# Optimization experiments

Measured on AMD Instinct MI355X. Metric: run time of the kernel, lower is better.

The kernel has to match this reference:

```python
import jax, jax.numpy as jnp
import numpy as np

B, L, DIN, H, E, K = 64, 256, 768, 64, 8, 2
S = 16  # sqrt(L): token<->feature grid side
LOSS_COEF = 1e-2


def gelu(x):
    return jax.nn.gelu(x, approximate=False)  # torch nn.GELU (exact erf)


def cv_squared(v):
    v = v.astype(jnp.float32)
    return jnp.var(v, ddof=1) / (jnp.mean(v) ** 2 + 1e-10)


def setup_inputs() -> dict:
    key = jax.random.key(0)
    ks = jax.random.split(key, 16)
    rn = lambda k, shape, s=0.02: jax.random.normal(k, shape, jnp.float32) * s
    lap = jnp.array([[0., 1., 0.], [1., -4., 1.], [0., 1., 0.]], jnp.float32)
    return {
        "x": jax.random.normal(ks[0], (B, L, DIN), jnp.float32),
        "dte": jax.random.normal(ks[1], (B, L, DIN), jnp.float32),
        "w_gate": rn(ks[2], (L, E), 1.0),
        "W_exp": rn(ks[3], (E, DIN, H)), "b_exp": jnp.zeros((E, H), jnp.float32),
        "W_sh": rn(ks[4], (DIN, H)), "b_sh": jnp.zeros((H,), jnp.float32),
        "ln_g": jnp.ones((H,), jnp.float32), "ln_b": jnp.zeros((H,), jnp.float32),
        "W_px": rn(ks[5], (H, 2 * H)), "b_px": jnp.zeros((2 * H,), jnp.float32),
        "conv_sh": jnp.tile(lap[None, None], (H, 1, 1, 1)),  # depthwise Laplacian [H,1,3,3]
        "W_pxx": rn(ks[6], (H, H)), "b_pxx": jnp.zeros((H,), jnp.float32),
        "W_dte": rn(ks[7], (H, H)), "b_dte": jnp.zeros((H,), jnp.float32),
        "W_dteall": rn(ks[8], (H, H)), "b_dteall": jnp.zeros((H,), jnp.float32),
        "W_rgb": rn(ks[9], (DIN, H)), "b_rgb": jnp.zeros((H,), jnp.float32),
        "W_fx": rn(ks[10], (H, H)), "b_fx": jnp.zeros((H,), jnp.float32),
        "W_fmod": rn(ks[11], (H, H)), "b_fmod": jnp.zeros((H,), jnp.float32),
        "W_fxx": rn(ks[12], (H, H)), "b_fxx": jnp.zeros((H,), jnp.float32),
    }


def reference(x, dte, w_gate, W_exp, b_exp, W_sh, b_sh, ln_g, ln_b, W_px, b_px,
              conv_sh, W_pxx, b_pxx, W_dte, b_dte, W_dteall, b_dteall,
              W_rgb, b_rgb, W_fx, b_fx, W_fmod, b_fmod, W_fxx, b_fxx):
    # ---- top-k gating (clean logits; noisy_gating=False / eval) ----
    logits = dte.mean(-1) @ w_gate                     # [B,E]
    topv, topi = jax.lax.top_k(logits, K)
    topg = jax.nn.softmax(topv, axis=1)
    gates = jnp.zeros_like(logits).at[jnp.arange(B)[:, None], topi].set(topg)
    importance = gates.sum(0)
    load = (gates > 0).sum(0).astype(jnp.float32)
    loss = LOSS_COEF * (cv_squared(importance) + cv_squared(load))
    # ---- sparse dispatch / expert Linear / weighted combine (dense-equivalent) ----
    y = jnp.einsum('be,bld,edh->blh', gates, dte, W_exp) + (gates @ b_exp)[:, None, :]
    # ---- shared expert Linear + Shared block ----
    sh = dte @ W_sh + b_sh                             # [B,L,H]
    shortcut = sh
    t = (sh - sh.mean(-1, keepdims=True)) * jax.lax.rsqrt(sh.var(-1, keepdims=True) + 1e-6)
    t = t * ln_g + ln_b
    t = t @ W_px + b_px                                # [B,L,2H]
    t1, t2 = t[..., :H], t[..., H:]
    f = t1.transpose(0, 2, 1).reshape(B, H, S, S)      # token2feature
    f = jax.lax.conv_general_dilated(f, conv_sh, (1, 1), 'SAME', feature_group_count=H)
    t1 = f.reshape(B, H, L).transpose(0, 2, 1)         # feature2token
    sh = (gelu(t1) * t2) @ W_pxx + b_pxx + shortcut
    # ---- combine MoE and shared streams ----
    dte_tok = (y @ W_dte + b_dte) + (sh @ W_dteall + b_dteall)
    rgb_tok = x @ W_rgb + b_rgb
    # ---- Fusion (its self.norm was overwritten to GELU; token<->feature round-trip is identity) ----
    shortcut = rgb_tok
    a = gelu(rgb_tok) @ W_fx + b_fx
    m = gelu(dte_tok) @ W_fmod + b_fmod
    out = (gelu(m) * a) @ W_fxx + b_fxx + shortcut     # [B,L,H]
    return out, loss
```

## Files before the change

### kernel.cpp

```cpp
#include <hip/hip_runtime.h>
#include <math.h>

typedef unsigned short u16;
typedef unsigned int u32;
typedef __attribute__((ext_vector_type(8))) short bf16x8;
typedef __attribute__((ext_vector_type(4))) float f32x4;


__device__ __forceinline__ float bf2f(u16 u) {
    union { u32 i; float f; } x; x.i = ((u32)u) << 16; return x.f;
}
__device__ __forceinline__ u16 f2bf(float f) {
    union { float f; u32 i; } x; x.f = f;
    u32 i = x.i;
    return (u16)((i + 0x7fffu + ((i >> 16) & 1u)) >> 16);
}
__device__ __forceinline__ u32 pack2(float a, float b) {
    return (u32)f2bf(a) | ((u32)f2bf(b) << 16);
}
__device__ __forceinline__ float wsum(float v) {
    #pragma unroll
    for (int o = 1; o < 64; o <<= 1) v += __shfl_xor(v, o, 64);
    return v;
}
__device__ __forceinline__ float gelu_f(float x) {
    return 0.5f * x * (1.0f + erff(x * 0.70710678118654752440f));
}

__global__ __launch_bounds__(256) void k_gate_part(const float* __restrict__ dte,
                                                   const float* __restrict__ w_gate,
                                                   float* __restrict__ partial) {
    __shared__ float dmeanS[64];
    int p = blockIdx.x, tid = threadIdx.x, w = tid >> 6, lane = tid & 63;
    for (int i = 0; i < 16; i++) {
        int l = w * 16 + i;
        const float* pr = dte + ((size_t)p * 64 + l) * 768;
        float s = 0.f;
        #pragma unroll
        for (int j = 0; j < 3; j++) {
            float4 v = *(const float4*)(pr + (lane + j * 64) * 4);
            s += v.x + v.y + v.z + v.w;
        }
        s = wsum(s);
        if (lane == 0) dmeanS[l] = s * (1.f / 768.f);
    }
    __syncthreads();
    if (w == 0) {
        float dm = dmeanS[lane];
        int wl = (p & 3) * 64 + lane;
        #pragma unroll
        for (int e = 0; e < 8; e++) {
            float s = wsum(dm * w_gate[wl * 8 + e]);
            if (lane == 0) partial[p * 8 + e] = s;
        }
    }
}

__global__ __launch_bounds__(256) void k_gate_fin(const float* __restrict__ partial,
                                                  const float* __restrict__ b_exp,
                                                  int* __restrict__ topi,
                                                  float* __restrict__ topg,
                                                  float* __restrict__ bias_y,
                                                  float* __restrict__ loss_out) {
    __shared__ float gS[64 * 8];
    __shared__ int i0S[64], i1S[64];
    __shared__ float g0S[64], g1S[64];
    int tid = threadIdx.x;
    if (tid < 64) {
        float lg[8];
        #pragma unroll
        for (int e = 0; e < 8; e++)
            lg[e] = partial[(tid * 4 + 0) * 8 + e] + partial[(tid * 4 + 1) * 8 + e] +
                    partial[(tid * 4 + 2) * 8 + e] + partial[(tid * 4 + 3) * 8 + e];
        int i0 = 0; float v0 = lg[0];
        #pragma unroll
        for (int e = 1; e < 8; e++) if (lg[e] > v0) { v0 = lg[e]; i0 = e; }
        int i1 = -1; float v1 = -1e30f;
        #pragma unroll
        for (int e = 0; e < 8; e++) if (e != i0 && lg[e] > v1) { v1 = lg[e]; i1 = e; }
        if (i1 < 0) i1 = (i0 + 1) & 7;
        float e2 = expf(v1 - v0);
        float g0 = 1.f / (1.f + e2);
        float g1 = e2 / (1.f + e2);
        #pragma unroll
        for (int e = 0; e < 8; e++) gS[tid * 8 + e] = 0.f;
        gS[tid * 8 + i0] = g0;
        gS[tid * 8 + i1] = g1;
        i0S[tid] = i0; i1S[tid] = i1; g0S[tid] = g0; g1S[tid] = g1;
        topi[tid * 2] = i0; topi[tid * 2 + 1] = i1;
        topg[tid * 2] = g0; topg[tid * 2 + 1] = g1;
    }
    __syncthreads();
    for (int idx = tid; idx < 4096; idx += 256) {
        int b = idx >> 6, h = idx & 63;
        bias_y[idx] = g0S[b] * b_exp[i0S[b] * 64 + h] + g1S[b] * b_exp[i1S[b] * 64 + h];
    }
    if (tid < 64) {
        float g[8];
        #pragma unroll
        for (int e = 0; e < 8; e++) g[e] = gS[tid * 8 + e];
        float imp[8], ld[8];
        #pragma unroll
        for (int e = 0; e < 8; e++) {
            imp[e] = wsum(g[e]);
            ld[e]  = wsum(g[e] > 0.f ? 1.f : 0.f);
        }
        if (tid == 0) {
            float l = 0.f;
            {
                float s = 0.f;
                #pragma unroll
                for (int e = 0; e < 8; e++) s += imp[e];
                float mn = s / 8.f, v = 0.f;
                #pragma unroll
                for (int e = 0; e < 8; e++) { float d = imp[e] - mn; v += d * d; }
                l += (v / 7.f) / (mn * mn + 1e-10f);
            }
            {
                float s = 0.f;
                #pragma unroll
                for (int e = 0; e < 8; e++) s += ld[e];
                float mn = s / 8.f, v = 0.f;
                #pragma unroll
                for (int e = 0; e < 8; e++) { float d = ld[e] - mn; v += d * d; }
                l += (v / 7.f) / (mn * mn + 1e-10f);
            }
            loss_out[0] = 0.01f * l;
        }
    }
}

__global__ __launch_bounds__(256) void k_gemm3(const float* __restrict__ dte,
                                               const float* __restrict__ x,
                                               const float* __restrict__ W_sh,
                                               const float* __restrict__ b_sh,
                                               const float* __restrict__ W_exp,
                                               const int* __restrict__ topi,
                                               const float* __restrict__ topg,
                                               const float* __restrict__ bias_y,
                                               const float* __restrict__ W_rgb,
                                               const float* __restrict__ b_rgb,
                                               float* __restrict__ buf_sh,
                                               u16* __restrict__ buf_y,
                                               float* __restrict__ out_rgb) {
    __shared__ u16 As[64 * 72];
    __shared__ u16 Wt[64 * 72];
    int bid = blockIdx.x;
    int kind, row0;
    if (bid < 512) { kind = bid & 1; row0 = (bid >> 1) * 64; }
    else           { kind = 2;       row0 = (bid - 512) * 64; }
    int b = row0 >> 8;
    int tid = threadIdx.x, wv = tid >> 6, lane = tid & 63;
    int m = lane & 15, quad = lane >> 4;

    const float* A = (kind == 2) ? x : dte;
    const float* W0 = (kind == 2) ? W_rgb : W_sh;
    const float* W1 = W0;
    float g0 = 0.f, g1 = 0.f;
    if (kind == 1) {
        W0 = W_exp + (size_t)topi[2 * b] * 49152;
        W1 = W_exp + (size_t)topi[2 * b + 1] * 49152;
        g0 = topg[2 * b]; g1 = topg[2 * b + 1];
    }

    float4 pa[2][2];
    float  pw[16];
    const int a_r  = tid >> 3;
    const int a_k8 = (tid & 7) * 8;
    const int w_n  = tid & 63;
    const int w_k0 = (tid >> 6) * 16;

    auto loadA = [&](int kc) {
        #pragma unroll
        for (int j = 0; j < 2; j++) {
            const float* src = A + (size_t)(row0 + a_r + j * 32) * 768 + kc * 64 + a_k8;
            pa[j][0] = *(const float4*)(src);
            pa[j][1] = *(const float4*)(src + 4);
        }
    };
    auto loadW = [&](int kc) {
        if (kind == 1) {
            #pragma unroll
            for (int j = 0; j < 16; j++) {
                size_t off = (size_t)(kc * 64 + w_k0 + j) * 64 + w_n;
                pw[j] = g0 * W0[off] + g1 * W1[off];
            }
        } else {
            #pragma unroll
            for (int j = 0; j < 16; j++)
                pw[j] = W0[(size_t)(kc * 64 + w_k0 + j) * 64 + w_n];
        }
    };
    auto stageLDS = [&]() {
        #pragma unroll
        for (int j = 0; j < 2; j++) {
            uint4 d;
            d.x = pack2(pa[j][0].x, pa[j][0].y);
            d.y = pack2(pa[j][0].z, pa[j][0].w);
            d.z = pack2(pa[j][1].x, pa[j][1].y);
            d.w = pack2(pa[j][1].z, pa[j][1].w);
            *(uint4*)&As[(a_r + j * 32) * 72 + a_k8] = d;
        }
        uint4 d0, d1;
        d0.x = pack2(pw[0],  pw[1]);  d0.y = pack2(pw[2],  pw[3]);
        d0.z = pack2(pw[4],  pw[5]);  d0.w = pack2(pw[6],  pw[7]);
        d1.x = pack2(pw[8],  pw[9]);  d1.y = pack2(pw[10], pw[11]);
        d1.z = pack2(pw[12], pw[13]); d1.w = pack2(pw[14], pw[15]);
        *(uint4*)&Wt[w_n * 72 + w_k0]     = d0;
        *(uint4*)&Wt[w_n * 72 + w_k0 + 8] = d1;
    };

    f32x4 acc0 = {0.f, 0.f, 0.f, 0.f}, acc1 = acc0, acc2 = acc0, acc3 = acc0;

    loadA(0); loadW(0);
    for (int kc = 0; kc < 12; kc++) {
        __syncthreads();
        stageLDS();
        __syncthreads();
        if (kc < 11) { loadA(kc + 1); loadW(kc + 1); }
        const int ar = (wv * 16 + m) * 72;
        bf16x8 a0 = *(const bf16x8*)&As[ar + quad * 8];
        bf16x8 a1 = *(const bf16x8*)&As[ar + 32 + quad * 8];
        #pragma unroll
        for (int t = 0; t < 4; t++) {
            const int br = (t * 16 + m) * 72;
            bf16x8 b0 = *(const bf16x8*)&Wt[br + quad * 8];
            bf16x8 b1 = *(const bf16x8*)&Wt[br + 32 + quad * 8];
            f32x4* accp = (t == 0) ? &acc0 : (t == 1) ? &acc1 : (t == 2) ? &acc2 : &acc3;
            *accp = __builtin_amdgcn_mfma_f32_16x16x32_bf16(a0, b0, *accp, 0, 0, 0);
            *accp = __builtin_amdgcn_mfma_f32_16x16x32_bf16(a1, b1, *accp, 0, 0, 0);
        }
    }

    f32x4 accs[4] = {acc0, acc1, acc2, acc3};
    #pragma unroll
    for (int t = 0; t < 4; t++) {
        int col = t * 16 + m;
        float bias;
        if (kind == 0)      bias = b_sh[col];
        else if (kind == 1) bias = bias_y[b * 64 + col];
        else                bias = b_rgb[col];
        #pragma unroll
        for (int i = 0; i < 4; i++) {
            int r = row0 + wv * 16 + quad * 4 + i;
            float val = accs[t][i] + bias;
            if (kind == 0)      buf_sh[(size_t)r * 64 + col] = val;
            else if (kind == 1) buf_y[(size_t)r * 64 + col] = f2bf(val);
            else                out_rgb[(size_t)r * 64 + col] = val;
        }
    }
}

__global__ __launch_bounds__(256) void k_lnpx(const float* __restrict__ buf_sh,
                                              const float* __restrict__ ln_g,
                                              const float* __restrict__ ln_b,
                                              const float* __restrict__ W_px,
                                              const float* __restrict__ b_px,
                                              u16* __restrict__ t1, u16* __restrict__ t2) {
    __shared__ float T[32 * 68];
    __shared__ float Wpx[8192];
    int r0 = blockIdx.x * 32;
    int tid = threadIdx.x, w = tid >> 6, lane = tid & 63;
    #pragma unroll
    for (int j = 0; j < 8; j++) {
        int e4 = tid + j * 256;
        *(float4*)(Wpx + e4 * 4) = *(const float4*)(W_px + e4 * 4);
    }
    float lnG = ln_g[lane], lnB = ln_b[lane];
    for (int i = 0; i < 8; i++) {
        int l = w * 8 + i;
        float v = buf_sh[(size_t)(r0 + l) * 64 + lane];
        float mean = wsum(v) * (1.f / 64.f);
        float d = v - mean;
        float var = wsum(d * d) * (1.f / 64.f);
        T[l * 68 + lane] = d * rsqrtf(var + 1e-6f) * lnG + lnB;
    }
    __syncthreads();
    int rg = tid >> 4, cg = tid & 15;
    float acc1[2][4] = {}, acc2[2][4] = {};
    const float* tr = T + rg * 2 * 68;
    #pragma unroll 4
    for (int kk = 0; kk < 64; kk++) {
        float a0 = tr[kk], a1 = tr[68 + kk];
        float4 w1 = *(const float4*)(Wpx + kk * 128 + cg * 4);
        float4 w2 = *(const float4*)(Wpx + kk * 128 + 64 + cg * 4);
        acc1[0][0] += a0 * w1.x; acc1[0][1] += a0 * w1.y; acc1[0][2] += a0 * w1.z; acc1[0][3] += a0 * w1.w;
        acc1[1][0] += a1 * w1.x; acc1[1][1] += a1 * w1.y; acc1[1][2] += a1 * w1.z; acc1[1][3] += a1 * w1.w;
        acc2[0][0] += a0 * w2.x; acc2[0][1] += a0 * w2.y; acc2[0][2] += a0 * w2.z; acc2[0][3] += a0 * w2.w;
        acc2[1][0] += a1 * w2.x; acc2[1][1] += a1 * w2.y; acc2[1][2] += a1 * w2.z; acc2[1][3] += a1 * w2.w;
    }
    float4 b1 = *(const float4*)(b_px + cg * 4);
    float4 b2 = *(const float4*)(b_px + 64 + cg * 4);
    #pragma unroll
    for (int i = 0; i < 2; i++) {
        int r = r0 + rg * 2 + i;
        u32* d1 = (u32*)(t1 + (size_t)r * 64 + cg * 4);
        d1[0] = pack2(acc1[i][0] + b1.x, acc1[i][1] + b1.y);
        d1[1] = pack2(acc1[i][2] + b1.z, acc1[i][3] + b1.w);
        u32* d2 = (u32*)(t2 + (size_t)r * 64 + cg * 4);
        d2[0] = pack2(acc2[i][0] + b2.x, acc2[i][1] + b2.y);
        d2[1] = pack2(acc2[i][2] + b2.z, acc2[i][3] + b2.w);
    }
}

__global__ __launch_bounds__(256) void k_tail(const u16* __restrict__ t1,
                                              const u16* __restrict__ t2,
                                              const float* __restrict__ conv_sh,
                                              const float* __restrict__ W_pxx,
                                              const float* __restrict__ b_pxx,
                                              const float* __restrict__ buf_sh,
                                              const u16* __restrict__ buf_y,
                                              const float* __restrict__ W_dte,
                                              const float* __restrict__ b_dte,
                                              const float* __restrict__ W_dteall,
                                              const float* __restrict__ b_dteall,
                                              const float* __restrict__ W_fx,
                                              const float* __restrict__ b_fx,
                                              const float* __restrict__ W_fmod,
                                              const float* __restrict__ b_fmod,
                                              const float* __restrict__ W_fxx,
                                              const float* __restrict__ b_fxx,
                                              float* __restrict__ out) {
    __shared__ float B0[32 * 68];
    __shared__ float B1[32 * 68];
    __shared__ float B2[32 * 68];
    __shared__ float RS[32 * 64];
    int r0 = blockIdx.x * 32;
    int tid = threadIdx.x, w = tid >> 6, lane = tid & 63;
    int rg = tid >> 4, cg = tid & 15;

    {
        float c0 = conv_sh[lane * 9 + 0], c1 = conv_sh[lane * 9 + 1], c2 = conv_sh[lane * 9 + 2];
        float c3 = conv_sh[lane * 9 + 3], c4 = conv_sh[lane * 9 + 4], c5 = conv_sh[lane * 9 + 5];
        float c6 = conv_sh[lane * 9 + 6], c7 = conv_sh[lane * 9 + 7], c8 = conv_sh[lane * 9 + 8];
        for (int i = 0; i < 8; i++) {
            int l = w * 8 + i;
            int gr = r0 + l;
            int pix = gr & 255, ii = pix >> 4, jj = pix & 15;
            const u16* p = t1 + (size_t)gr * 64 + lane;
            float c = c4 * bf2f(p[0]);
            if (ii > 0) {
                c += c1 * bf2f(p[-1024]);
                if (jj > 0)  c += c0 * bf2f(p[-1024 - 64]);
                if (jj < 15) c += c2 * bf2f(p[-1024 + 64]);
            }
            if (jj > 0)  c += c3 * bf2f(p[-64]);
            if (jj < 15) c += c5 * bf2f(p[64]);
            if (ii < 15) {
                c += c7 * bf2f(p[1024]);
                if (jj > 0)  c += c6 * bf2f(p[1024 - 64]);
                if (jj < 15) c += c8 * bf2f(p[1024 + 64]);
            }
            B0[l * 68 + lane] = gelu_f(c) * bf2f(t2[(size_t)gr * 64 + lane]);
        }
    }
    __syncthreads();

    {
        float acc[2][4] = {};
        const float* ur = B0 + rg * 2 * 68;
        #pragma unroll 8
        for (int kk = 0; kk < 64; kk++) {
            float a0 = ur[kk], a1 = ur[68 + kk];
            float4 wvv = *(const float4*)(W_pxx + kk * 64 + cg * 4);
            acc[0][0] += a0 * wvv.x; acc[0][1] += a0 * wvv.y; acc[0][2] += a0 * wvv.z; acc[0][3] += a0 * wvv.w;
            acc[1][0] += a1 * wvv.x; acc[1][1] += a1 * wvv.y; acc[1][2] += a1 * wvv.z; acc[1][3] += a1 * wvv.w;
        }
        float4 bp = *(const float4*)(b_pxx + cg * 4);
        #pragma unroll
        for (int i = 0; i < 2; i++) {
            int lr = rg * 2 + i;
            float4 shv = *(const float4*)(buf_sh + (size_t)(r0 + lr) * 64 + cg * 4);
            *(float4*)(B1 + lr * 68 + cg * 4) =
                make_float4(acc[i][0] + bp.x + shv.x, acc[i][1] + bp.y + shv.y,
                            acc[i][2] + bp.z + shv.z, acc[i][3] + bp.w + shv.w);
        }
    }
    __syncthreads();

    #pragma unroll
    for (int j = 0; j < 8; j++) {
        int e = tid + j * 256;
        int l = e >> 6, c = e & 63;
        B0[l * 68 + c] = bf2f(buf_y[(size_t)(r0 + l) * 64 + c]);
    }
    __syncthreads();

    {
        float acc[2][4] = {};
        const float* yr = B0 + rg * 2 * 68;
        const float* sr = B1 + rg * 2 * 68;
        #pragma unroll 4
        for (int kk = 0; kk < 64; kk++) {
            float y0 = yr[kk], y1 = yr[68 + kk];
            float s0 = sr[kk], s1 = sr[68 + kk];
            float4 w1 = *(const float4*)(W_dte + kk * 64 + cg * 4);
            float4 w2 = *(const float4*)(W_dteall + kk * 64 + cg * 4);
            acc[0][0] += y0 * w1.x + s0 * w2.x; acc[0][1] += y0 * w1.y + s0 * w2.y;
            acc[0][2] += y0 * w1.z + s0 * w2.z; acc[0][3] += y0 * w1.w + s0 * w2.w;
            acc[1][0] += y1 * w1.x + s1 * w2.x; acc[1][1] += y1 * w1.y + s1 * w2.y;
            acc[1][2] += y1 * w1.z + s1 * w2.z; acc[1][3] += y1 * w1.w + s1 * w2.w;
        }
        float4 bd1 = *(const float4*)(b_dte + cg * 4);
        float4 bd2 = *(const float4*)(b_dteall + cg * 4);
        #pragma unroll
        for (int i = 0; i < 2; i++) {
            int lr = rg * 2 + i;
            *(float4*)(B2 + lr * 68 + cg * 4) =
                make_float4(gelu_f(acc[i][0] + bd1.x + bd2.x), gelu_f(acc[i][1] + bd1.y + bd2.y),
                            gelu_f(acc[i][2] + bd1.z + bd2.z), gelu_f(acc[i][3] + bd1.w + bd2.w));
        }
    }
    __syncthreads();

    #pragma unroll
    for (int j = 0; j < 2; j++) {
        int e4 = tid + j * 256;
        int l = e4 >> 4, c4i = e4 & 15;
        float4 rv = *(const float4*)(out + (size_t)(r0 + l) * 64 + c4i * 4);
        *(float4*)(RS + l * 64 + c4i * 4) = rv;
        B1[l * 68 + c4i * 4 + 0] = gelu_f(rv.x);
        B1[l * 68 + c4i * 4 + 1] = gelu_f(rv.y);
        B1[l * 68 + c4i * 4 + 2] = gelu_f(rv.z);
        B1[l * 68 + c4i * 4 + 3] = gelu_f(rv.w);
    }
    __syncthreads();

    {
        float accA[2][4] = {}, accM[2][4] = {};
        const float* ga = B1 + rg * 2 * 68;
        const float* gm = B2 + rg * 2 * 68;
        #pragma unroll 4
        for (int kk = 0; kk < 64; kk++) {
            float a0 = ga[kk], a1 = ga[68 + kk];
            float m0 = gm[kk], m1 = gm[68 + kk];
            float4 wa = *(const float4*)(W_fx + kk * 64 + cg * 4);
            float4 wm = *(const float4*)(W_fmod + kk * 64 + cg * 4);
            accA[0][0] += a0 * wa.x; accA[0][1] += a0 * wa.y; accA[0][2] += a0 * wa.z; accA[0][3] += a0 * wa.w;
            accA[1][0] += a1 * wa.x; accA[1][1] += a1 * wa.y; accA[1][2] += a1 * wa.z; accA[1][3] += a1 * wa.w;
            accM[0][0] += m0 * wm.x; accM[0][1] += m0 * wm.y; accM[0][2] += m0 * wm.z; accM[0][3] += m0 * wm.w;
            accM[1][0] += m1 * wm.x; accM[1][1] += m1 * wm.y; accM[1][2] += m1 * wm.z; accM[1][3] += m1 * wm.w;
        }
        float4 bx = *(const float4*)(b_fx + cg * 4);
        float4 bm = *(const float4*)(b_fmod + cg * 4);
        #pragma unroll
        for (int i = 0; i < 2; i++) {
            int lr = rg * 2 + i;
            float a0 = accA[i][0] + bx.x, a1 = accA[i][1] + bx.y, a2 = accA[i][2] + bx.z, a3 = accA[i][3] + bx.w;
            float m0 = accM[i][0] + bm.x, m1 = accM[i][1] + bm.y, m2 = accM[i][2] + bm.z, m3 = accM[i][3] + bm.w;
            *(float4*)(B0 + lr * 68 + cg * 4) =
                make_float4(gelu_f(m0) * a0, gelu_f(m1) * a1, gelu_f(m2) * a2, gelu_f(m3) * a3);
        }
    }
    __syncthreads();

    {
        float acc[2][4] = {};
        const float* pr = B0 + rg * 2 * 68;
        #pragma unroll 8
        for (int kk = 0; kk < 64; kk++) {
            float p0 = pr[kk], p1 = pr[68 + kk];
            float4 wvv = *(const float4*)(W_fxx + kk * 64 + cg * 4);
            acc[0][0] += p0 * wvv.x; acc[0][1] += p0 * wvv.y; acc[0][2] += p0 * wvv.z; acc[0][3] += p0 * wvv.w;
            acc[1][0] += p1 * wvv.x; acc[1][1] += p1 * wvv.y; acc[1][2] += p1 * wvv.z; acc[1][3] += p1 * wvv.w;
        }
        float4 bo = *(const float4*)(b_fxx + cg * 4);
        #pragma unroll
        for (int i = 0; i < 2; i++) {
            int lr = rg * 2 + i;
            *(float4*)(out + (size_t)(r0 + lr) * 64 + cg * 4) =
                make_float4(acc[i][0] + bo.x + RS[lr * 64 + cg * 4 + 0],
                            acc[i][1] + bo.y + RS[lr * 64 + cg * 4 + 1],
                            acc[i][2] + bo.z + RS[lr * 64 + cg * 4 + 2],
                            acc[i][3] + bo.w + RS[lr * 64 + cg * 4 + 3]);
        }
    }
}

extern "C" void kernel_launch(void* const* d_in, const int* in_sizes, int n_in,
                              void* d_out, int out_size, void* d_ws, size_t ws_size,
                              hipStream_t stream) {
    const float* x       = (const float*)d_in[0];
    const float* dte     = (const float*)d_in[1];
    const float* w_gate  = (const float*)d_in[2];
    const float* W_exp   = (const float*)d_in[3];
    const float* b_exp   = (const float*)d_in[4];
    const float* W_sh    = (const float*)d_in[5];
    const float* b_sh    = (const float*)d_in[6];
    const float* ln_g    = (const float*)d_in[7];
    const float* ln_b    = (const float*)d_in[8];
    const float* W_px    = (const float*)d_in[9];
    const float* b_px    = (const float*)d_in[10];
    const float* conv_sh = (const float*)d_in[11];
    const float* W_pxx   = (const float*)d_in[12];
    const float* b_pxx   = (const float*)d_in[13];
    const float* W_dte   = (const float*)d_in[14];
    const float* b_dte   = (const float*)d_in[15];
    const float* W_dteall= (const float*)d_in[16];
    const float* b_dteall= (const float*)d_in[17];
    const float* W_rgb   = (const float*)d_in[18];
    const float* b_rgb   = (const float*)d_in[19];
    const float* W_fx    = (const float*)d_in[20];
    const float* b_fx    = (const float*)d_in[21];
    const float* W_fmod  = (const float*)d_in[22];
    const float* b_fmod  = (const float*)d_in[23];
    const float* W_fxx   = (const float*)d_in[24];
    const float* b_fxx   = (const float*)d_in[25];

    float* out = (float*)d_out;

    float* wsf    = (float*)d_ws;
    float* partial= wsf;
    int*   topi   = (int*)(wsf + 2048);
    float* topg   = wsf + 2176;
    float* bias_y = wsf + 2304;
    float* buf_sh = wsf + 8192;
    u16*   buf_y  = (u16*)(wsf + 8192 + 1048576);
    u16*   t1     = (u16*)(wsf + 8192 + 1048576 + 524288);
    u16*   t2     = (u16*)(wsf + 8192 + 1048576 + 524288*2);

    hipLaunchKernelGGL(k_gate_part, dim3(256), dim3(256), 0, stream, dte, w_gate, partial);
    hipLaunchKernelGGL(k_gate_fin, dim3(1), dim3(256), 0, stream,
                       partial, b_exp, topi, topg, bias_y, out + 1048576);
    hipLaunchKernelGGL(k_gemm3, dim3(768), dim3(256), 0, stream,
                       dte, x, W_sh, b_sh, W_exp, topi, topg, bias_y, W_rgb, b_rgb,
                       buf_sh, buf_y, out);
    hipLaunchKernelGGL(k_lnpx, dim3(512), dim3(256), 0, stream,
                       buf_sh, ln_g, ln_b, W_px, b_px, t1, t2);
    hipLaunchKernelGGL(k_tail, dim3(512), dim3(256), 0, stream,
                       t1, t2, conv_sh, W_pxx, b_pxx, buf_sh, buf_y,
                       W_dte, b_dte, W_dteall, b_dteall,
                       W_fx, b_fx, W_fmod, b_fmod, W_fxx, b_fxx, out);

    (void)in_sizes; (void)n_in; (void)out_size; (void)ws_size;
}
```

Before: 252.6 us.

## Double-buffer tail weights in LDS via async global_load_lds and split GEMM stages

The tail kernel now stages each 64x64 weight matrix into LDS with asynchronous global-to-LDS loads, double-buffered, so the next matrix loads while the current small GEMM runs. Before, every thread read the weights straight from global memory inside the inner loop. The fused two-matrix GEMMs are split into separate single-matrix passes. The residual and the y input are preloaded into registers and LDS (y kept as bf16) at kernel start, which removes extra barrier phases. This raises LDS use to about 60KB per block, which may lower occupancy, and it relies on the async loads completing before each barrier.

```diff
diff --git a/kernel.cpp b/kernel.cpp
--- a/kernel.cpp
+++ b/kernel.cpp
@@ -321,18 +321,48 @@
                                               const float* __restrict__ W_fxx,
                                               const float* __restrict__ b_fxx,
                                               float* __restrict__ out) {
-    __shared__ float B0[32 * 68];
-    __shared__ float B1[32 * 68];
-    __shared__ float B2[32 * 68];
-    __shared__ float RS[32 * 64];
+    __shared__ float C0[32 * 68];
+    __shared__ float GA[32 * 68];
+    __shared__ float SH1[32 * 68];
+    __shared__ float GM[32 * 68];
+    __shared__ u16   Ybh[32 * 72];
+    __shared__ __align__(16) float WL[2][4096];
     int r0 = blockIdx.x * 32;
     int tid = threadIdx.x, w = tid >> 6, lane = tid & 63;
     int rg = tid >> 4, cg = tid & 15;
 
+    auto stage_w = [&](const float* __restrict__ Wsrc, int half) {
+        const float* g = Wsrc + w * 1024 + lane * 4;
+        float* l = &WL[half][w * 1024];
+        #pragma unroll
+        for (int j = 0; j < 4; j++) {
+            __builtin_amdgcn_global_load_lds(
+                (const __attribute__((address_space(1))) unsigned int*)(g + j * 256),
+                (__attribute__((address_space(3))) unsigned int*)(l + j * 256),
+                16, 0, 0);
+        }
+    };
+
+    stage_w(W_pxx, 0);
+
+    stage_w(W_dte, 1);
+    float4 rsv[2];
+    #pragma unroll
+    for (int i = 0; i < 2; i++) {
+        int r = rg * 2 + i;
+        uint2 v = *(const uint2*)(buf_y + (size_t)(r0 + r) * 64 + cg * 4);
+        *(uint2*)(&Ybh[r * 72 + cg * 4]) = v;
+        rsv[i] = *(const float4*)(out + (size_t)(r0 + r) * 64 + cg * 4);
+        GA[r * 68 + cg * 4 + 0] = gelu_f(rsv[i].x);
+        GA[r * 68 + cg * 4 + 1] = gelu_f(rsv[i].y);
+        GA[r * 68 + cg * 4 + 2] = gelu_f(rsv[i].z);
+        GA[r * 68 + cg * 4 + 3] = gelu_f(rsv[i].w);
+    }
     {
         float c0 = conv_sh[lane * 9 + 0], c1 = conv_sh[lane * 9 + 1], c2 = conv_sh[lane * 9 + 2];
         float c3 = conv_sh[lane * 9 + 3], c4 = conv_sh[lane * 9 + 4], c5 = conv_sh[lane * 9 + 5];
         float c6 = conv_sh[lane * 9 + 6], c7 = conv_sh[lane * 9 + 7], c8 = conv_sh[lane * 9 + 8];
+        #pragma unroll
         for (int i = 0; i < 8; i++) {
             int l = w * 8 + i;
             int gr = r0 + l;
@@ -351,104 +381,102 @@
                 if (jj > 0)  c += c6 * bf2f(p[1024 - 64]);
                 if (jj < 15) c += c8 * bf2f(p[1024 + 64]);
             }
-            B0[l * 68 + lane] = gelu_f(c) * bf2f(t2[(size_t)gr * 64 + lane]);
+            C0[l * 68 + lane] = gelu_f(c) * bf2f(t2[(size_t)gr * 64 + lane]);
         }
     }
     __syncthreads();
 
     {
         float acc[2][4] = {};
-        const float* ur = B0 + rg * 2 * 68;
+        const float* ur = C0 + rg * 2 * 68;
         #pragma unroll 8
         for (int kk = 0; kk < 64; kk++) {
             float a0 = ur[kk], a1 = ur[68 + kk];
-            float4 wvv = *(const float4*)(W_pxx + kk * 64 + cg * 4);
-            acc[0][0] += a0 * wvv.x; acc[0][1] += a0 * wvv.y; acc[0][2] += a0 * wvv.z; acc[0][3] += a0 * wvv.w;
-            acc[1][0] += a1 * wvv.x; acc[1][1] += a1 * wvv.y; acc[1][2] += a1 * wvv.z; acc[1][3] += a1 * wvv.w;
+            float4 wv = *(const float4*)(&WL[0][kk * 64 + cg * 4]);
+            acc[0][0] += a0 * wv.x; acc[0][1] += a0 * wv.y; acc[0][2] += a0 * wv.z; acc[0][3] += a0 * wv.w;
+            acc[1][0] += a1 * wv.x; acc[1][1] += a1 * wv.y; acc[1][2] += a1 * wv.z; acc[1][3] += a1 * wv.w;
         }
         float4 bp = *(const float4*)(b_pxx + cg * 4);
         #pragma unroll
         for (int i = 0; i < 2; i++) {
-            int lr = rg * 2 + i;
-            float4 shv = *(const float4*)(buf_sh + (size_t)(r0 + lr) * 64 + cg * 4);
-            *(float4*)(B1 + lr * 68 + cg * 4) =
+            int r = rg * 2 + i;
+            float4 shv = *(const float4*)(buf_sh + (size_t)(r0 + r) * 64 + cg * 4);
+            *(float4*)(SH1 + r * 68 + cg * 4) =
                 make_float4(acc[i][0] + bp.x + shv.x, acc[i][1] + bp.y + shv.y,
                             acc[i][2] + bp.z + shv.z, acc[i][3] + bp.w + shv.w);
         }
     }
     __syncthreads();
 
-    #pragma unroll
-    for (int j = 0; j < 8; j++) {
-        int e = tid + j * 256;
-        int l = e >> 6, c = e & 63;
-        B0[l * 68 + c] = bf2f(buf_y[(size_t)(r0 + l) * 64 + c]);
-    }
-    __syncthreads();
-
-    {
-        float acc[2][4] = {};
-        const float* yr = B0 + rg * 2 * 68;
-        const float* sr = B1 + rg * 2 * 68;
-        #pragma unroll 4
+    float accC[2][4] = {};
+    stage_w(W_dteall, 0);
+    {
+        const u16* yr = Ybh + rg * 2 * 72;
+        #pragma unroll 8
         for (int kk = 0; kk < 64; kk++) {
-            float y0 = yr[kk], y1 = yr[68 + kk];
+            float y0 = bf2f(yr[kk]), y1 = bf2f(yr[72 + kk]);
+            float4 wv = *(const float4*)(&WL[1][kk * 64 + cg * 4]);
+            accC[0][0] += y0 * wv.x; accC[0][1] += y0 * wv.y; accC[0][2] += y0 * wv.z; accC[0][3] += y0 * wv.w;
+            accC[1][0] += y1 * wv.x; accC[1][1] += y1 * wv.y; accC[1][2] += y1 * wv.z; accC[1][3] += y1 * wv.w;
+        }
+    }
+    __syncthreads();
+
+    stage_w(W_fx, 1);
+    {
+        const float* sr = SH1 + rg * 2 * 68;
+        #pragma unroll 8
+        for (int kk = 0; kk < 64; kk++) {
             float s0 = sr[kk], s1 = sr[68 + kk];
-            float4 w1 = *(const float4*)(W_dte + kk * 64 + cg * 4);
-            float4 w2 = *(const float4*)(W_dteall + kk * 64 + cg * 4);
-            acc[0][0] += y0 * w1.x + s0 * w2.x; acc[0][1] += y0 * w1.y + s0 * w2.y;
-            acc[0][2] += y0 * w1.z + s0 * w2.z; acc[0][3] += y0 * w1.w + s0 * w2.w;
-            acc[1][0] += y1 * w1.x + s1 * w2.x; acc[1][1] += y1 * w1.y + s1 * w2.y;
-            acc[1][2] += y1 * w1.z + s1 * w2.z; acc[1][3] += y1 * w1.w + s1 * w2.w;
+            float4 wv = *(const float4*)(&WL[0][kk * 64 + cg * 4]);
+            accC[0][0] += s0 * wv.x; accC[0][1] += s0 * wv.y; accC[0][2] += s0 * wv.z; accC[0][3] += s0 * wv.w;
+            accC[1][0] += s1 * wv.x; accC[1][1] += s1 * wv.y; accC[1][2] += s1 * wv.z; accC[1][3] += s1 * wv.w;
         }
         float4 bd1 = *(const float4*)(b_dte + cg * 4);
         float4 bd2 = *(const float4*)(b_dteall + cg * 4);
         #pragma unroll
         for (int i = 0; i < 2; i++) {
-            int lr = rg * 2 + i;
-            *(float4*)(B2 + lr * 68 + cg * 4) =
-                make_float4(gelu_f(acc[i][0] + bd1.x + bd2.x), gelu_f(acc[i][1] + bd1.y + bd2.y),
-                            gelu_f(acc[i][2] + bd1.z + bd2.z), gelu_f(acc[i][3] + bd1.w + bd2.w));
-        }
-    }
-    __syncthreads();
-
-    #pragma unroll
-    for (int j = 0; j < 2; j++) {
-        int e4 = tid + j * 256;
-        int l = e4 >> 4, c4i = e4 & 15;
-        float4 rv = *(const float4*)(out + (size_t)(r0 + l) * 64 + c4i * 4);
-        *(float4*)(RS + l * 64 + c4i * 4) = rv;
-        B1[l * 68 + c4i * 4 + 0] = gelu_f(rv.x);
-        B1[l * 68 + c4i * 4 + 1] = gelu_f(rv.y);
-        B1[l * 68 + c4i * 4 + 2] = gelu_f(rv.z);
-        B1[l * 68 + c4i * 4 + 3] = gelu_f(rv.w);
-    }
-    __syncthreads();
-
-    {
-        float accA[2][4] = {}, accM[2][4] = {};
-        const float* ga = B1 + rg * 2 * 68;
-        const float* gm = B2 + rg * 2 * 68;
-        #pragma unroll 4
+            int r = rg * 2 + i;
+            *(float4*)(GM + r * 68 + cg * 4) =
+                make_float4(gelu_f(accC[i][0] + bd1.x + bd2.x), gelu_f(accC[i][1] + bd1.y + bd2.y),
+                            gelu_f(accC[i][2] + bd1.z + bd2.z), gelu_f(accC[i][3] + bd1.w + bd2.w));
+        }
+    }
+    __syncthreads();
+
+    float accA[2][4] = {};
+    stage_w(W_fmod, 0);
+    {
+        const float* ga = GA + rg * 2 * 68;
+        #pragma unroll 8
         for (int kk = 0; kk < 64; kk++) {
             float a0 = ga[kk], a1 = ga[68 + kk];
+            float4 wv = *(const float4*)(&WL[1][kk * 64 + cg * 4]);
+            accA[0][0] += a0 * wv.x; accA[0][1] += a0 * wv.y; accA[0][2] += a0 * wv.z; accA[0][3] += a0 * wv.w;
+            accA[1][0] += a1 * wv.x; accA[1][1] += a1 * wv.y; accA[1][2] += a1 * wv.z; accA[1][3] += a1 * wv.w;
+        }
+    }
+    __syncthreads();
+
+    stage_w(W_fxx, 1);
+    {
+        float accM[2][4] = {};
+        const float* gm = GM + rg * 2 * 68;
+        #pragma unroll 8
+        for (int kk = 0; kk < 64; kk++) {
             float m0 = gm[kk], m1 = gm[68 + kk];
-            float4 wa = *(const float4*)(W_fx + kk * 64 + cg * 4);
-            float4 wm = *(const float4*)(W_fmod + kk * 64 + cg * 4);
-            accA[0][0] += a0 * wa.x; accA[0][1] += a0 * wa.y; accA[0][2] += a0 * wa.z; accA[0][3] += a0 * wa.w;
-            accA[1][0] += a1 * wa.x; accA[1][1] += a1 * wa.y; accA[1][2] += a1 * wa.z; accA[1][3] += a1 * wa.w;
-            accM[0][0] += m0 * wm.x; accM[0][1] += m0 * wm.y; accM[0][2] += m0 * wm.z; accM[0][3] += m0 * wm.w;
-            accM[1][0] += m1 * wm.x; accM[1][1] += m1 * wm.y; accM[1][2] += m1 * wm.z; accM[1][3] += m1 * wm.w;
+            float4 wv = *(const float4*)(&WL[0][kk * 64 + cg * 4]);
+            accM[0][0] += m0 * wv.x; accM[0][1] += m0 * wv.y; accM[0][2] += m0 * wv.z; accM[0][3] += m0 * wv.w;
+            accM[1][0] += m1 * wv.x; accM[1][1] += m1 * wv.y; accM[1][2] += m1 * wv.z; accM[1][3] += m1 * wv.w;
         }
         float4 bx = *(const float4*)(b_fx + cg * 4);
         float4 bm = *(const float4*)(b_fmod + cg * 4);
         #pragma unroll
         for (int i = 0; i < 2; i++) {
-            int lr = rg * 2 + i;
+            int r = rg * 2 + i;
             float a0 = accA[i][0] + bx.x, a1 = accA[i][1] + bx.y, a2 = accA[i][2] + bx.z, a3 = accA[i][3] + bx.w;
             float m0 = accM[i][0] + bm.x, m1 = accM[i][1] + bm.y, m2 = accM[i][2] + bm.z, m3 = accM[i][3] + bm.w;
-            *(float4*)(B0 + lr * 68 + cg * 4) =
+            *(float4*)(C0 + r * 68 + cg * 4) =
                 make_float4(gelu_f(m0) * a0, gelu_f(m1) * a1, gelu_f(m2) * a2, gelu_f(m3) * a3);
         }
     }
@@ -456,23 +484,21 @@
 
     {
         float acc[2][4] = {};
-        const float* pr = B0 + rg * 2 * 68;
+        const float* pr = C0 + rg * 2 * 68;
         #pragma unroll 8
         for (int kk = 0; kk < 64; kk++) {
             float p0 = pr[kk], p1 = pr[68 + kk];
-            float4 wvv = *(const float4*)(W_fxx + kk * 64 + cg * 4);
-            acc[0][0] += p0 * wvv.x; acc[0][1] += p0 * wvv.y; acc[0][2] += p0 * wvv.z; acc[0][3] += p0 * wvv.w;
-            acc[1][0] += p1 * wvv.x; acc[1][1] += p1 * wvv.y; acc[1][2] += p1 * wvv.z; acc[1][3] += p1 * wvv.w;
+            float4 wv = *(const float4*)(&WL[1][kk * 64 + cg * 4]);
+            acc[0][0] += p0 * wv.x; acc[0][1] += p0 * wv.y; acc[0][2] += p0 * wv.z; acc[0][3] += p0 * wv.w;
+            acc[1][0] += p1 * wv.x; acc[1][1] += p1 * wv.y; acc[1][2] += p1 * wv.z; acc[1][3] += p1 * wv.w;
         }
         float4 bo = *(const float4*)(b_fxx + cg * 4);
         #pragma unroll
         for (int i = 0; i < 2; i++) {
-            int lr = rg * 2 + i;
-            *(float4*)(out + (size_t)(r0 + lr) * 64 + cg * 4) =
-                make_float4(acc[i][0] + bo.x + RS[lr * 64 + cg * 4 + 0],
-                            acc[i][1] + bo.y + RS[lr * 64 + cg * 4 + 1],
-                            acc[i][2] + bo.z + RS[lr * 64 + cg * 4 + 2],
-                            acc[i][3] + bo.w + RS[lr * 64 + cg * 4 + 3]);
+            int r = rg * 2 + i;
+            *(float4*)(out + (size_t)(r0 + r) * 64 + cg * 4) =
+                make_float4(acc[i][0] + bo.x + rsv[i].x, acc[i][1] + bo.y + rsv[i].y,
+                            acc[i][2] + bo.z + rsv[i].z, acc[i][3] + bo.w + rsv[i].w);
         }
     }
 }
```

Result: faster. 242.2 us (-4.1%).
